# Kernel tuning notes

Hardware: AMD Instinct MI355X
Metric: run time of the kernel (lower is better)

The kernel has to match this reference:

```python
import jax, jax.numpy as jnp
import numpy as np

B = 65536      # batch (e.g. edges)
U = 128        # channel multiplicity of irreps_in1
SQRT2 = 1.4142135623730951
SQRT3 = 1.7320508075688772

# Levi-Civita tensor eps[i,j,k]
_eps = np.zeros((3, 3, 3), dtype=np.float32)
_eps[0, 1, 2] = _eps[1, 2, 0] = _eps[2, 0, 1] = 1.0
_eps[0, 2, 1] = _eps[2, 1, 0] = _eps[1, 0, 2] = -1.0
EPS = jnp.asarray(_eps)


def setup_inputs() -> dict:
    key = jax.random.key(0)
    k1, k2, k3 = jax.random.split(key, 3)
    x1 = jax.random.normal(k1, (B, 4 * U), dtype=jnp.float32)   # 128x0e + 128x1o, mul_ir layout
    x2 = jax.random.normal(k2, (B, 4), dtype=jnp.float32)       # 1x0e + 1x1o
    weight = jax.random.normal(k3, (1, 5 * U), dtype=jnp.float32)  # 5 paths * u(128) * v(1)
    return {"x1": x1, "x2": x2, "weight": weight}


def reference(x1, x2, weight):
    """Channel-wise tensor product: out[k,u*v] = sum_ij CG[i,j,k] w[u,v] x1[i,u] x2[j,v].
    mul_ir layout: each irrep segment stored as (mul, 2l+1) flattened."""
    b = x1.shape[0]
    s0 = x1[:, :U]                       # (B, U)    0e segment
    s1 = x1[:, U:].reshape(b, U, 3)      # (B, U, 3) 1o segment
    y0 = x2[:, 0]                        # (B,)      0e
    y1 = x2[:, 1:4]                      # (B, 3)    1o
    w = weight.reshape(5, U)             # shared weights, one u-vector per path

    # path 0: 0e x 0e -> 0e   (CG = 1)
    o0 = w[0] * s0 * y0[:, None]                                        # (B, U)
    # path 1: 0e x 1o -> 1o   (CG = delta_jk after component norm)
    o1 = w[1][None, :, None] * s0[:, :, None] * y1[:, None, :]          # (B, U, 3)
    # path 2: 1o x 0e -> 1o   (CG = delta_ik)
    o2 = w[2][None, :, None] * s1 * y0[:, None, None]                   # (B, U, 3)
    # path 3: 1o x 1o -> 0e   (CG = delta_ij / sqrt(3))
    o3 = w[3] * jnp.einsum('bui,bi->bu', s1, y1) / SQRT3                # (B, U)
    # path 4: 1o x 1o -> 1e   (CG = eps_ijk / sqrt(2) after component norm)
    o4 = w[4][None, :, None] * jnp.einsum('ijk,bui,bj->buk', EPS, s1, y1) / SQRT2  # (B, U, 3)

    # concatenate output segments in mul_ir layout (path order)
    return jnp.concatenate(
        [o0, o1.reshape(b, 3 * U), o2.reshape(b, 3 * U), o3, o4.reshape(b, 3 * U)],
        axis=1,
    )  # (B, 11*U)


if __name__ == "__main__":
    out = reference(**setup_inputs())
    print(out.shape, out.dtype)
```

## Files before the change

kernel.cpp:

```cpp
#include <hip/hip_runtime.h>

namespace {

constexpr int U = 128;
constexpr float INV_SQRT3 = 0.57735026918962576f;
constexpr float INV_SQRT2 = 0.70710678118654752f;

struct F3 { float x, y, z; };

__global__ __launch_bounds__(256) void tp_kernel(
    const float* __restrict__ x1, const float* __restrict__ x2,
    const float* __restrict__ w, float* __restrict__ out, int nrows) {
  const int t = blockIdx.x * blockDim.x + threadIdx.x;
  const int b = t >> 7;
  const int u = t & (U - 1);
  if (b >= nrows) return;

  const float* x1row = x1 + (size_t)b * (4 * U);
  const float s0 = x1row[u];
  const F3 s1 = reinterpret_cast<const F3*>(x1row + U)[u];
  const float4 y = reinterpret_cast<const float4*>(x2)[b];

  const float w0 = w[u];
  const float w1 = w[U + u];
  const float w2 = w[2 * U + u];
  const float w3 = w[3 * U + u];
  const float w4 = w[4 * U + u];

  float* orow = out + (size_t)b * (11 * U);

  orow[u] = w0 * s0 * y.x;

  const float t1 = w1 * s0;
  reinterpret_cast<F3*>(orow + U)[u] = {t1 * y.y, t1 * y.z, t1 * y.w};

  const float t2 = w2 * y.x;
  reinterpret_cast<F3*>(orow + 4 * U)[u] = {t2 * s1.x, t2 * s1.y, t2 * s1.z};

  orow[7 * U + u] =
      w3 * (s1.x * y.y + s1.y * y.z + s1.z * y.w) * INV_SQRT3;

  const float c0 = s1.y * y.w - s1.z * y.z;
  const float c1 = s1.z * y.y - s1.x * y.w;
  const float c2 = s1.x * y.z - s1.y * y.y;
  const float t4 = w4 * INV_SQRT2;
  reinterpret_cast<F3*>(orow + 8 * U)[u] = {t4 * c0, t4 * c1, t4 * c2};
}

}

extern "C" void kernel_launch(void* const* d_in, const int* in_sizes, int n_in,
                              void* d_out, int out_size, void* d_ws, size_t ws_size,
                              hipStream_t stream) {
  const float* x1 = (const float*)d_in[0];
  const float* x2 = (const float*)d_in[1];
  const float* w  = (const float*)d_in[2];
  float* out = (float*)d_out;

  const int nrows = in_sizes[0] / (4 * U);
  const int total = nrows * U;
  const int block = 256;
  const int grid = (total + block - 1) / block;

  hipLaunchKernelGGL(tp_kernel, dim3(grid), dim3(block), 0, stream,
                     x1, x2, w, out, nrows);
}
```

Before: 446.0 us.

## Stage rows through shared memory for coalesced float4 loads and stores

Each block now handles 4 rows. It copies the input rows into LDS with float4 loads, computes all paths into an LDS output buffer, then writes the output rows back with coalesced float4 stores. This replaces the strided 12-byte F3 global accesses and is meant to raise the efficiency of global memory transactions. The cost is about 30KB of LDS per block, which limits occupancy, plus two barriers and possible LDS bank conflicts on the stride-3 accesses.

```diff
diff --git a/kernel.cpp b/kernel.cpp
--- a/kernel.cpp
+++ b/kernel.cpp
@@ -3,48 +3,77 @@
 namespace {
 
 constexpr int U = 128;
+constexpr int ROW_IN = 4 * U;
+constexpr int ROW_OUT = 11 * U;
+constexpr int R = 4;
 constexpr float INV_SQRT3 = 0.57735026918962576f;
 constexpr float INV_SQRT2 = 0.70710678118654752f;
-
-struct F3 { float x, y, z; };
 
 __global__ __launch_bounds__(256) void tp_kernel(
     const float* __restrict__ x1, const float* __restrict__ x2,
     const float* __restrict__ w, float* __restrict__ out, int nrows) {
-  const int t = blockIdx.x * blockDim.x + threadIdx.x;
-  const int b = t >> 7;
-  const int u = t & (U - 1);
-  if (b >= nrows) return;
+  __shared__ float sin_[R * ROW_IN];
+  __shared__ float sout[R * ROW_OUT];
 
-  const float* x1row = x1 + (size_t)b * (4 * U);
-  const float s0 = x1row[u];
-  const F3 s1 = reinterpret_cast<const F3*>(x1row + U)[u];
-  const float4 y = reinterpret_cast<const float4*>(x2)[b];
+  const int tid = threadIdx.x;
+  const int row0 = blockIdx.x * R;
+  const int rows_here = min(R, nrows - row0);
+  if (rows_here <= 0) return;
 
+  {
+    const float4* g = reinterpret_cast<const float4*>(x1 + (size_t)row0 * ROW_IN);
+    float4* s = reinterpret_cast<float4*>(sin_);
+    const int n4 = rows_here * (ROW_IN / 4);
+    for (int idx = tid; idx < n4; idx += 256) s[idx] = g[idx];
+  }
+
+  const int u = tid & (U - 1);
   const float w0 = w[u];
   const float w1 = w[U + u];
   const float w2 = w[2 * U + u];
   const float w3 = w[3 * U + u];
   const float w4 = w[4 * U + u];
 
-  float* orow = out + (size_t)b * (11 * U);
+  __syncthreads();
 
-  orow[u] = w0 * s0 * y.x;
+  const int rr = tid >> 7;
+#pragma unroll
+  for (int p = 0; p < R / 2; ++p) {
+    const int r = 2 * p + rr;
+    if (r < rows_here) {
+      const float* xr = sin_ + r * ROW_IN;
+      const float s0 = xr[u];
+      const float s1x = xr[U + 3 * u];
+      const float s1y = xr[U + 3 * u + 1];
+      const float s1z = xr[U + 3 * u + 2];
+      const float4 y = reinterpret_cast<const float4*>(x2)[row0 + r];
 
-  const float t1 = w1 * s0;
-  reinterpret_cast<F3*>(orow + U)[u] = {t1 * y.y, t1 * y.z, t1 * y.w};
+      float* o = sout + r * ROW_OUT;
+      o[u] = w0 * s0 * y.x;
+      const float t1 = w1 * s0;
+      o[U + 3 * u] = t1 * y.y;
+      o[U + 3 * u + 1] = t1 * y.z;
+      o[U + 3 * u + 2] = t1 * y.w;
+      const float t2 = w2 * y.x;
+      o[4 * U + 3 * u] = t2 * s1x;
+      o[4 * U + 3 * u + 1] = t2 * s1y;
+      o[4 * U + 3 * u + 2] = t2 * s1z;
+      o[7 * U + u] = w3 * (s1x * y.y + s1y * y.z + s1z * y.w) * INV_SQRT3;
+      const float t4 = w4 * INV_SQRT2;
+      o[8 * U + 3 * u] = t4 * (s1y * y.w - s1z * y.z);
+      o[8 * U + 3 * u + 1] = t4 * (s1z * y.y - s1x * y.w);
+      o[8 * U + 3 * u + 2] = t4 * (s1x * y.z - s1y * y.y);
+    }
+  }
 
-  const float t2 = w2 * y.x;
-  reinterpret_cast<F3*>(orow + 4 * U)[u] = {t2 * s1.x, t2 * s1.y, t2 * s1.z};
+  __syncthreads();
 
-  orow[7 * U + u] =
-      w3 * (s1.x * y.y + s1.y * y.z + s1.z * y.w) * INV_SQRT3;
-
-  const float c0 = s1.y * y.w - s1.z * y.z;
-  const float c1 = s1.z * y.y - s1.x * y.w;
-  const float c2 = s1.x * y.z - s1.y * y.y;
-  const float t4 = w4 * INV_SQRT2;
-  reinterpret_cast<F3*>(orow + 8 * U)[u] = {t4 * c0, t4 * c1, t4 * c2};
+  {
+    float4* g = reinterpret_cast<float4*>(out + (size_t)row0 * ROW_OUT);
+    const float4* s = reinterpret_cast<const float4*>(sout);
+    const int n4 = rows_here * (ROW_OUT / 4);
+    for (int idx = tid; idx < n4; idx += 256) g[idx] = s[idx];
+  }
 }
 
 }
@@ -58,9 +87,8 @@
   float* out = (float*)d_out;
 
   const int nrows = in_sizes[0] / (4 * U);
-  const int total = nrows * U;
+  const int grid = (nrows + R - 1) / R;
   const int block = 256;
-  const int grid = (total + block - 1) / block;
 
   hipLaunchKernelGGL(tp_kernel, dim3(grid), dim3(block), 0, stream,
                      x1, x2, w, out, nrows);
```

After: 445.6 us. About the same (-0.1%).
